# Optimization experiments

Measured on AMD Instinct MI355X. Metric: run time of the kernel, lower is better.

The kernel has to match this reference:

```python
import jax, jax.numpy as jnp
import numpy as np

D_MODEL = 1024
NHEAD = 16
HEAD_DIM = D_MODEL // NHEAD  # 64
AXIS_DIM = HEAD_DIM // 4     # 16
DFF = 4096
EPS = 1e-5
BASE = 10000.0
B, S = 4, 2048


def setup_inputs() -> dict:
    key = jax.random.key(0)
    ks = jax.random.split(key, 10)
    def xavier(k, shape):
        fan_in, fan_out = shape[1], shape[0]
        limit = np.sqrt(6.0 / (fan_in + fan_out))
        return jax.random.uniform(k, shape, jnp.float32, -limit, limit)
    return {
        "src": jax.random.normal(ks[0], (B, S, D_MODEL), jnp.float32),
        "positions": jax.random.normal(ks[1], (B, S, 4), jnp.float32),
        "w_qkv": xavier(ks[2], (3 * D_MODEL, D_MODEL)),
        "w_out": xavier(ks[3], (D_MODEL, D_MODEL)),
        "norm1_w": jnp.ones((D_MODEL,), jnp.float32),
        "norm2_w": jnp.ones((D_MODEL,), jnp.float32),
        "w1": xavier(ks[4], (DFF, D_MODEL)),
        "w2": xavier(ks[5], (D_MODEL, DFF)),
        "w3": xavier(ks[6], (DFF, D_MODEL)),
        "axis_scale": jnp.ones((4,), jnp.float32),
    }


def _rmsnorm(x, w, eps=EPS):
    return x * jax.lax.rsqrt(jnp.mean(x * x, axis=-1, keepdims=True) + eps) * w


def _rope_rotate(x, cos, sin):
    # x: (B,H,S,HEAD_DIM); cos/sin: (B,1,S,4,AXIS_DIM//2)
    b, h, s, _ = x.shape
    xr = x.reshape(b, h, s, 4, AXIS_DIM // 2, 2)  # 4 axis chunks, interleaved pairs
    e, o = xr[..., 0], xr[..., 1]
    re = e * cos - o * sin
    ro = o * cos + e * sin
    return jnp.stack([re, ro], axis=-1).reshape(b, h, s, HEAD_DIM)


def reference(src, positions, w_qkv, w_out, norm1_w, norm2_w, w1, w2, w3, axis_scale):
    b, s, _ = src.shape
    x = src
    x_norm = _rmsnorm(x, norm1_w)
    qkv = x_norm @ w_qkv.T  # (B,S,3*D)
    qkv = qkv.reshape(b, s, 3, NHEAD, HEAD_DIM).transpose(2, 0, 3, 1, 4)
    q, k, v = qkv[0], qkv[1], qkv[2]  # (B,H,S,Dh)

    # 4D RoPE: same inv_freq per axis (base^{-idx/axis_dim})
    inv_freq = BASE ** (-(jnp.arange(0, AXIS_DIM, 2, dtype=jnp.float32) / AXIS_DIM))  # (8,)
    coord = positions * axis_scale  # (B,S,4)
    angles = coord[..., None] * inv_freq  # (B,S,4,8)
    cos = jnp.cos(angles)[:, None]  # (B,1,S,4,8)
    sin = jnp.sin(angles)[:, None]
    q = _rope_rotate(q, cos, sin)
    k = _rope_rotate(k, cos, sin)

    scale = 1.0 / jnp.sqrt(jnp.float32(HEAD_DIM))
    scores = jnp.einsum("bhqd,bhkd->bhqk", q, k) * scale
    attn = jax.nn.softmax(scores, axis=-1)
    attn_out = jnp.einsum("bhqk,bhkd->bhqd", attn, v)
    attn_out = attn_out.transpose(0, 2, 1, 3).reshape(b, s, D_MODEL)
    x = x + attn_out @ w_out.T

    x_norm = _rmsnorm(x, norm2_w)
    ff = (jax.nn.silu(x_norm @ w1.T) * (x_norm @ w3.T)) @ w2.T
    return x + ff
```

## Files before the change

kernel.cpp:

```cpp
#include <hip/hip_runtime.h>

typedef unsigned short u16;
typedef __attribute__((ext_vector_type(4))) unsigned short u16x4;
typedef __attribute__((ext_vector_type(8))) short bf16x8;
typedef __attribute__((ext_vector_type(4))) float f32x4;
typedef __attribute__((ext_vector_type(16))) float f32x16;

__device__ __forceinline__ float bf2f(u16 u) {
  union { unsigned i; float f; } v; v.i = ((unsigned)u) << 16; return v.f;
}
__device__ __forceinline__ u16 f2bf(float f) {
  union { float f; unsigned i; } v; v.f = f;
  unsigned r = v.i + 0x7fffu + ((v.i >> 16) & 1u);
  return (u16)(r >> 16);
}
__device__ __forceinline__ void gl_lds16(const u16* g, u16* l) {
  __builtin_amdgcn_global_load_lds((const __attribute__((address_space(1))) unsigned*)g,
                                   (__attribute__((address_space(3))) unsigned*)l, 16, 0, 0);
}
__device__ __forceinline__ f32x16 mfma32(bf16x8 a, bf16x8 b, f32x16 c) {
  return __builtin_amdgcn_mfma_f32_32x32x16_bf16(a, b, c, 0, 0, 0);
}

__global__ __launch_bounds__(256) void k_cvt(const float* __restrict__ S,
                                             u16* __restrict__ D, int n) {
  int i = (blockIdx.x * 256 + threadIdx.x) * 8;
  if (i >= n) return;
  f32x4 a = *(const f32x4*)(S + i), b = *(const f32x4*)(S + i + 4);
  bf16x8 r;
  r[0] = (short)f2bf(a.x); r[1] = (short)f2bf(a.y); r[2] = (short)f2bf(a.z); r[3] = (short)f2bf(a.w);
  r[4] = (short)f2bf(b.x); r[5] = (short)f2bf(b.y); r[6] = (short)f2bf(b.z); r[7] = (short)f2bf(b.w);
  *(bf16x8*)(D + i) = r;
}

__global__ __launch_bounds__(256) void k_rmsnorm(const void* __restrict__ X,
                                                 const float* __restrict__ W,
                                                 u16* __restrict__ Y, int x_ext) {
  const int tok = blockIdx.x, t = threadIdx.x;
  float x0, x1, x2, x3;
  if (x_ext) {
    f32x4 xv = ((const f32x4*)X)[tok * 256 + t];
    x0 = xv.x; x1 = xv.y; x2 = xv.z; x3 = xv.w;
  } else {
    u16x4 xv = ((const u16x4*)X)[tok * 256 + t];
    x0 = bf2f(xv.x); x1 = bf2f(xv.y); x2 = bf2f(xv.z); x3 = bf2f(xv.w);
  }
  float ss = x0 * x0 + x1 * x1 + x2 * x2 + x3 * x3;
#pragma unroll
  for (int m = 32; m; m >>= 1) ss += __shfl_xor(ss, m);
  __shared__ float red[4];
  if ((t & 63) == 0) red[t >> 6] = ss;
  __syncthreads();
  float inv = rsqrtf((red[0] + red[1] + red[2] + red[3]) * (1.f / 1024.f) + 1e-5f);
  f32x4 wv = ((const f32x4*)W)[t];
  u16x4 o;
  o.x = f2bf(x0 * inv * wv.x);
  o.y = f2bf(x1 * inv * wv.y);
  o.z = f2bf(x2 * inv * wv.z);
  o.w = f2bf(x3 * inv * wv.w);
  ((u16x4*)(Y + (size_t)tok * 1024))[t] = o;
}

template <int EPI, int OUTF32>
__global__ __launch_bounds__(256, 2) void k_gemm(const u16* __restrict__ A,
                                                 const u16* __restrict__ W,
                                                 const void* R, void* C,
                                                 int M, int N, int K, int r_ext) {
  __shared__ u16 sA[128 * 32];
  __shared__ u16 sB[128 * 32];
  const int t = threadIdx.x;
  const int wid = t >> 6, lane = t & 63, quad = lane >> 4, l16 = lane & 15;
  const int wm = wid >> 1, wn = wid & 1;
  const size_t m0 = (size_t)blockIdx.y * 128, n0 = (size_t)blockIdx.x * 128;
  f32x4 acc[4][4] = {};
  const int srow = t >> 2, schunk = t & 3;
  const u16* Ag = A + (m0 + srow) * K + schunk * 8;
  const u16* Wg = W + (n0 + srow) * (size_t)K + schunk * 8;
  u16* sAw = sA + wid * 512;
  u16* sBw = sB + wid * 512;
  for (int k0 = 0; k0 < K; k0 += 32) {
    gl_lds16(Ag + k0, sAw);
    gl_lds16(Ag + (size_t)64 * K + k0, sAw + 2048);
    gl_lds16(Wg + k0, sBw);
    gl_lds16(Wg + (size_t)64 * K + k0, sBw + 2048);
    __syncthreads();
    bf16x8 a[4], b[4];
#pragma unroll
    for (int mt = 0; mt < 4; ++mt)
      a[mt] = *(const bf16x8*)(sA + (wm * 64 + mt * 16 + l16) * 32 + quad * 8);
#pragma unroll
    for (int nt = 0; nt < 4; ++nt)
      b[nt] = *(const bf16x8*)(sB + (wn * 64 + nt * 16 + l16) * 32 + quad * 8);
#pragma unroll
    for (int mt = 0; mt < 4; ++mt)
#pragma unroll
      for (int nt = 0; nt < 4; ++nt)
        acc[mt][nt] = __builtin_amdgcn_mfma_f32_16x16x32_bf16(a[mt], b[nt], acc[mt][nt], 0, 0, 0);
    __syncthreads();
  }
#pragma unroll
  for (int mt = 0; mt < 4; ++mt) {
#pragma unroll
    for (int nt = 0; nt < 4; ++nt) {
      size_t row = m0 + wm * 64 + mt * 16 + quad * 4;
      size_t col = n0 + wn * 64 + nt * 16 + l16;
#pragma unroll
      for (int r = 0; r < 4; ++r) {
        float v = acc[mt][nt][r];
        size_t idx = (row + r) * N + col;
        if (EPI == 1) v += r_ext ? ((const float*)R)[idx] : bf2f(((const u16*)R)[idx]);
        if (OUTF32) ((float*)C)[idx] = v;
        else ((u16*)C)[idx] = f2bf(v);
      }
    }
  }
}

__global__ __launch_bounds__(256, 2) void k_ffn(const u16* __restrict__ A,
                                                const u16* __restrict__ W1,
                                                const u16* __restrict__ W3,
                                                u16* __restrict__ C,
                                                int M, int N, int K) {
  __shared__ u16 sA[128 * 32];
  __shared__ u16 sB1[128 * 32];
  __shared__ u16 sB3[128 * 32];
  const int t = threadIdx.x;
  const int wid = t >> 6, lane = t & 63, quad = lane >> 4, l16 = lane & 15;
  const int wm = wid >> 1, wn = wid & 1;
  const size_t m0 = (size_t)blockIdx.y * 128, n0 = (size_t)blockIdx.x * 128;
  f32x4 acc1[4][4] = {};
  f32x4 acc3[4][4] = {};
  const int srow = t >> 2, schunk = t & 3;
  const u16* Ag = A + (m0 + srow) * K + schunk * 8;
  const u16* W1g = W1 + (n0 + srow) * (size_t)K + schunk * 8;
  const u16* W3g = W3 + (n0 + srow) * (size_t)K + schunk * 8;
  u16* sAw = sA + wid * 512;
  u16* sB1w = sB1 + wid * 512;
  u16* sB3w = sB3 + wid * 512;
  for (int k0 = 0; k0 < K; k0 += 32) {
    gl_lds16(Ag + k0, sAw);
    gl_lds16(Ag + (size_t)64 * K + k0, sAw + 2048);
    gl_lds16(W1g + k0, sB1w);
    gl_lds16(W1g + (size_t)64 * K + k0, sB1w + 2048);
    gl_lds16(W3g + k0, sB3w);
    gl_lds16(W3g + (size_t)64 * K + k0, sB3w + 2048);
    __syncthreads();
    bf16x8 a[4], b1[4], b3[4];
#pragma unroll
    for (int mt = 0; mt < 4; ++mt)
      a[mt] = *(const bf16x8*)(sA + (wm * 64 + mt * 16 + l16) * 32 + quad * 8);
#pragma unroll
    for (int nt = 0; nt < 4; ++nt) {
      b1[nt] = *(const bf16x8*)(sB1 + (wn * 64 + nt * 16 + l16) * 32 + quad * 8);
      b3[nt] = *(const bf16x8*)(sB3 + (wn * 64 + nt * 16 + l16) * 32 + quad * 8);
    }
#pragma unroll
    for (int mt = 0; mt < 4; ++mt)
#pragma unroll
      for (int nt = 0; nt < 4; ++nt) {
        acc1[mt][nt] = __builtin_amdgcn_mfma_f32_16x16x32_bf16(a[mt], b1[nt], acc1[mt][nt], 0, 0, 0);
        acc3[mt][nt] = __builtin_amdgcn_mfma_f32_16x16x32_bf16(a[mt], b3[nt], acc3[mt][nt], 0, 0, 0);
      }
    __syncthreads();
  }
#pragma unroll
  for (int mt = 0; mt < 4; ++mt) {
#pragma unroll
    for (int nt = 0; nt < 4; ++nt) {
      size_t row = m0 + wm * 64 + mt * 16 + quad * 4;
      size_t col = n0 + wn * 64 + nt * 16 + l16;
#pragma unroll
      for (int r = 0; r < 4; ++r) {
        float v1 = acc1[mt][nt][r];
        float v3 = acc3[mt][nt][r];
        float h = v1 / (1.f + __expf(-v1)) * v3;
        C[(row + r) * N + col] = f2bf(h);
      }
    }
  }
}

__global__ __launch_bounds__(256) void k_rope(const u16* __restrict__ QKV,
                                              const float* __restrict__ POS,
                                              const float* __restrict__ ASC,
                                              u16* __restrict__ Qr, u16* __restrict__ Kr,
                                              u16* __restrict__ Vt) {
  const int bh = blockIdx.x, b = bh >> 4, h = bh & 15;
  const int s0 = blockIdx.y * 128;
  const int t = threadIdx.x;
  const int pr = t & 31, a = pr >> 3, f = pr & 7, srow = t >> 5;
  const float asc = ASC[a];
  const float invf = exp2f(-(float)f * (13.28771237954945f / 8.f));
  for (int pass = 0; pass < 16; ++pass) {
    int s = s0 + pass * 8 + srow;
    float ang = POS[((size_t)b * 2048 + s) * 4 + a] * asc * invf;
    float sn, cs;
    sincosf(ang, &sn, &cs);
    size_t ib = ((size_t)b * 2048 + s) * 3072 + h * 64 + a * 16 + f * 2;
    size_t ob = ((size_t)bh * 2048 + s) * 64 + a * 16 + f * 2;
    unsigned qw = *(const unsigned*)(QKV + ib);
    float e = bf2f((u16)(qw & 0xffff)), o = bf2f((u16)(qw >> 16));
    *(unsigned*)(Qr + ob) = (unsigned)f2bf(e * cs - o * sn) | ((unsigned)f2bf(o * cs + e * sn) << 16);
    unsigned kw = *(const unsigned*)(QKV + ib + 1024);
    e = bf2f((u16)(kw & 0xffff));
    o = bf2f((u16)(kw >> 16));
    *(unsigned*)(Kr + ob) = (unsigned)f2bf(e * cs - o * sn) | ((unsigned)f2bf(o * cs + e * sn) << 16);
  }
  __shared__ u16 vt[64 * 130];
#pragma unroll
  for (int it = 0; it < 32; ++it) {
    int idx = it * 256 + t, sl = idx >> 6, d = idx & 63;
    vt[d * 130 + sl] = QKV[((size_t)b * 2048 + s0 + sl) * 3072 + 2048 + h * 64 + d];
  }
  __syncthreads();
#pragma unroll
  for (int it = 0; it < 32; ++it) {
    int idx = it * 256 + t, d = idx >> 7, sl = idx & 127;
    Vt[((size_t)bh * 64 + d) * 2048 + s0 + sl] = vt[d * 130 + sl];
  }
}

#define SCL 0.18033688011112042f

__global__ __launch_bounds__(256, 2) void k_attn(const u16* __restrict__ Qr,
                                                 const u16* __restrict__ Kr,
                                                 const u16* __restrict__ Vt,
                                                 u16* __restrict__ O) {
  __shared__ u16 sK[2][4096];
  __shared__ u16 sV[2][4096];
  const int t = threadIdx.x, wid = t >> 6, lane = t & 63;
  const int il = lane & 31, hh = lane >> 5;
  const int bh = blockIdx.x;
  const int q0 = blockIdx.y * 256 + wid * 64;
  const size_t base = (size_t)bh * 2048 * 64;

  bf16x8 qf[2][4];
#pragma unroll
  for (int qt = 0; qt < 2; ++qt)
#pragma unroll
    for (int c = 0; c < 4; ++c)
      qf[qt][c] = *(const bf16x8*)(Qr + base + (size_t)(q0 + qt * 32 + il) * 64 + c * 16 + hh * 8);

  const f32x16 ZERO = {};
  f32x16 oa[2][2] = {{ZERO, ZERO}, {ZERO, ZERO}};
  float m[2] = {-1e30f, -1e30f}, lr[2] = {0.f, 0.f};

  const u16* Kb = Kr + base;
  const u16* Vb = Vt + base;
  const int cc = t & 7, r0 = t >> 3;
  {
    bf16x8 k0 = *(const bf16x8*)(Kb + (size_t)r0 * 64 + cc * 8);
    bf16x8 k1 = *(const bf16x8*)(Kb + (size_t)(r0 + 32) * 64 + cc * 8);
    bf16x8 v0 = *(const bf16x8*)(Vb + (size_t)r0 * 2048 + cc * 8);
    bf16x8 v1 = *(const bf16x8*)(Vb + (size_t)(r0 + 32) * 2048 + cc * 8);
    *(bf16x8*)(sK[0] + (cc * 64 + (r0 ^ cc)) * 8) = k0;
    *(bf16x8*)(sK[0] + (cc * 64 + ((r0 + 32) ^ cc)) * 8) = k1;
    *(bf16x8*)(sV[0] + (cc * 64 + (r0 ^ cc)) * 8) = v0;
    *(bf16x8*)(sV[0] + (cc * 64 + ((r0 + 32) ^ cc)) * 8) = v1;
  }
  __syncthreads();

  for (int it = 0; it < 32; ++it) {
    const u16* kb = sK[it & 1];
    const u16* vb = sV[it & 1];
    bf16x8 nk0, nk1, nv0, nv1;
    const int last = (it == 31);
    if (!last) {
      int kv = (it + 1) * 64;
      nk0 = *(const bf16x8*)(Kb + (size_t)(kv + r0) * 64 + cc * 8);
      nk1 = *(const bf16x8*)(Kb + (size_t)(kv + r0 + 32) * 64 + cc * 8);
      nv0 = *(const bf16x8*)(Vb + (size_t)r0 * 2048 + kv + cc * 8);
      nv1 = *(const bf16x8*)(Vb + (size_t)(r0 + 32) * 2048 + kv + cc * 8);
    }
    f32x16 sacc[2][2];
    __builtin_amdgcn_s_setprio(1);
#pragma unroll
    for (int kt = 0; kt < 2; ++kt) {
#pragma unroll
      for (int c = 0; c < 4; ++c) {
        int ch = c * 2 + hh;
        bf16x8 kf = *(const bf16x8*)(kb + (ch * 64 + ((kt * 32 + il) ^ ch)) * 8);
        if (c == 0) {
          sacc[0][kt] = mfma32(kf, qf[0][0], ZERO);
          sacc[1][kt] = mfma32(kf, qf[1][0], ZERO);
        } else {
          sacc[0][kt] = mfma32(kf, qf[0][c], sacc[0][kt]);
          sacc[1][kt] = mfma32(kf, qf[1][c], sacc[1][kt]);
        }
      }
    }
    __builtin_amdgcn_s_setprio(0);
    bf16x8 pa[2][4];
#pragma unroll
    for (int qt = 0; qt < 2; ++qt) {
      float mx = -1e30f;
#pragma unroll
      for (int kt = 0; kt < 2; ++kt)
#pragma unroll
        for (int r = 0; r < 16; ++r) mx = fmaxf(mx, sacc[qt][kt][r]);
      mx = fmaxf(mx, __shfl_xor(mx, 32));
      if (!__all(mx - m[qt] <= 64.f)) {
        float mn = fmaxf(m[qt], mx);
        float corr = exp2f((m[qt] - mn) * SCL);
        m[qt] = mn;
        lr[qt] *= corr;
#pragma unroll
        for (int dt = 0; dt < 2; ++dt)
#pragma unroll
          for (int r = 0; r < 16; ++r) oa[qt][dt][r] *= corr;
      }
      float mm = m[qt];
#pragma unroll
      for (int kt = 0; kt < 2; ++kt) {
        float p[16];
        float ls = 0.f;
#pragma unroll
        for (int r = 0; r < 16; ++r) {
          p[r] = exp2f((sacc[qt][kt][r] - mm) * SCL);
          ls += p[r];
        }
        lr[qt] += ls;
        unsigned w[8];
#pragma unroll
        for (int i = 0; i < 8; ++i)
          asm("v_cvt_pk_bf16_f32 %0, %1, %2" : "=v"(w[i]) : "v"(p[2 * i]), "v"(p[2 * i + 1]));
        asm("v_permlane32_swap_b32 %0, %1" : "+v"(w[0]), "+v"(w[2]));
        asm("v_permlane32_swap_b32 %0, %1" : "+v"(w[1]), "+v"(w[3]));
        asm("v_permlane32_swap_b32 %0, %1" : "+v"(w[4]), "+v"(w[6]));
        asm("v_permlane32_swap_b32 %0, %1" : "+v"(w[5]), "+v"(w[7]));
        union { unsigned u[4]; bf16x8 v; } f0, f1;
        f0.u[0] = w[0]; f0.u[1] = w[1]; f0.u[2] = w[2]; f0.u[3] = w[3];
        f1.u[0] = w[4]; f1.u[1] = w[5]; f1.u[2] = w[6]; f1.u[3] = w[7];
        pa[qt][kt * 2] = f0.v;
        pa[qt][kt * 2 + 1] = f1.v;
      }
    }
    __builtin_amdgcn_s_setprio(1);
#pragma unroll
    for (int ks = 0; ks < 4; ++ks) {
      int sc = ks * 2 + hh;
#pragma unroll
      for (int dt = 0; dt < 2; ++dt) {
        bf16x8 vf = *(const bf16x8*)(vb + (sc * 64 + ((dt * 32 + il) ^ sc)) * 8);
        oa[0][dt] = mfma32(vf, pa[0][ks], oa[0][dt]);
        oa[1][dt] = mfma32(vf, pa[1][ks], oa[1][dt]);
      }
    }
    __builtin_amdgcn_s_setprio(0);
    if (!last) {
      u16* kn = sK[(it + 1) & 1];
      u16* vn = sV[(it + 1) & 1];
      *(bf16x8*)(kn + (cc * 64 + (r0 ^ cc)) * 8) = nk0;
      *(bf16x8*)(kn + (cc * 64 + ((r0 + 32) ^ cc)) * 8) = nk1;
      *(bf16x8*)(vn + (cc * 64 + (r0 ^ cc)) * 8) = nv0;
      *(bf16x8*)(vn + (cc * 64 + ((r0 + 32) ^ cc)) * 8) = nv1;
    }
    __syncthreads();
  }
  const int b = bh >> 4, hd = bh & 15;
#pragma unroll
  for (int qt = 0; qt < 2; ++qt) {
    float lt = lr[qt] + __shfl_xor(lr[qt], 32);
    float inv = 1.f / lt;
    int q = q0 + qt * 32 + il;
#pragma unroll
    for (int dt = 0; dt < 2; ++dt) {
#pragma unroll
      for (int g = 0; g < 4; ++g) {
        u16x4 pk;
        pk.x = f2bf(oa[qt][dt][4 * g + 0] * inv);
        pk.y = f2bf(oa[qt][dt][4 * g + 1] * inv);
        pk.z = f2bf(oa[qt][dt][4 * g + 2] * inv);
        pk.w = f2bf(oa[qt][dt][4 * g + 3] * inv);
        *(u16x4*)(O + ((size_t)b * 2048 + q) * 1024 + hd * 64 + dt * 32 + 8 * g + 4 * hh) = pk;
      }
    }
  }
}

extern "C" void kernel_launch(void* const* d_in, const int* in_sizes, int n_in,
                              void* d_out, int out_size, void* d_ws, size_t ws_size,
                              hipStream_t stream) {
  const float* src    = (const float*)d_in[0];
  const float* pos    = (const float*)d_in[1];
  const float* w_qkv  = (const float*)d_in[2];
  const float* w_out  = (const float*)d_in[3];
  const float* n1w    = (const float*)d_in[4];
  const float* n2w    = (const float*)d_in[5];
  const float* w1     = (const float*)d_in[6];
  const float* w2     = (const float*)d_in[7];
  const float* w3     = (const float*)d_in[8];
  const float* ascale = (const float*)d_in[9];
  char* ws = (char*)d_ws;
  u16* xn  = (u16*)(ws);
  u16* qkv = (u16*)(ws + ((size_t)16 << 20));
  u16* Qr  = (u16*)(ws);
  u16* Kr  = (u16*)(ws + ((size_t)64 << 20));
  u16* Vt  = (u16*)(ws + ((size_t)80 << 20));
  u16* att = (u16*)(ws + ((size_t)16 << 20));
  u16* x   = (u16*)(ws + ((size_t)80 << 20));
  u16* xn2 = (u16*)(ws);
  u16* h1  = (u16*)(ws + ((size_t)16 << 20));
  u16* bqkv = (u16*)(ws + ((size_t)96 << 20));
  u16* bout = (u16*)(ws + ((size_t)102 << 20));
  u16* b1   = (u16*)(ws + ((size_t)104 << 20));
  u16* b3   = (u16*)(ws + ((size_t)112 << 20));
  u16* b2   = (u16*)(ws + ((size_t)120 << 20));

  k_cvt<<<1536, 256, 0, stream>>>(w_qkv, bqkv, 3145728);
  k_cvt<<<512,  256, 0, stream>>>(w_out, bout, 1048576);
  k_cvt<<<2048, 256, 0, stream>>>(w1, b1, 4194304);
  k_cvt<<<2048, 256, 0, stream>>>(w3, b3, 4194304);
  k_cvt<<<2048, 256, 0, stream>>>(w2, b2, 4194304);

  k_rmsnorm<<<8192, 256, 0, stream>>>(src, n1w, xn, 1);
  k_gemm<0, 0><<<dim3(24, 64), 256, 0, stream>>>(xn, bqkv, nullptr, qkv, 8192, 3072, 1024, 0);
  k_rope<<<dim3(64, 16), 256, 0, stream>>>(qkv, pos, ascale, Qr, Kr, Vt);
  k_attn<<<dim3(64, 8), 256, 0, stream>>>(Qr, Kr, Vt, att);
  k_gemm<1, 0><<<dim3(8, 64), 256, 0, stream>>>(att, bout, src, x, 8192, 1024, 1024, 1);
  k_rmsnorm<<<8192, 256, 0, stream>>>(x, n2w, xn2, 0);
  k_ffn<<<dim3(32, 64), 256, 0, stream>>>(xn2, b1, b3, h1, 8192, 4096, 1024);
  k_gemm<1, 1><<<dim3(8, 64), 256, 0, stream>>>(h1, b2, x, d_out, 8192, 1024, 4096, 0);
}
```

Measured before the change: 699.5 us.

## Halve attention query tile per wave and reorganize GEMM LDS staging layout

The attention kernel now gives each wave 32 queries instead of 64 and launches twice as many blocks, raising the occupancy hint from 2 to 4 blocks per CU. The row max and row sum are now computed with tree reductions. The GEMM and FFN kernels change the global-to-LDS load mapping so that each wave stages whole 16-row MFMA tiles contiguously, which makes the fragment reads linear per lane and avoids strided LDS bank conflicts. The attention change trades fewer registers and more parallelism for half the reuse of each K/V tile per block, which means more LDS loads and K/V traffic.

```diff
diff --git a/kernel.cpp b/kernel.cpp
--- a/kernel.cpp
+++ b/kernel.cpp
@@ -73,9 +73,8 @@
   const int wm = wid >> 1, wn = wid & 1;
   const size_t m0 = (size_t)blockIdx.y * 128, n0 = (size_t)blockIdx.x * 128;
   f32x4 acc[4][4] = {};
-  const int srow = t >> 2, schunk = t & 3;
-  const u16* Ag = A + (m0 + srow) * K + schunk * 8;
-  const u16* Wg = W + (n0 + srow) * (size_t)K + schunk * 8;
+  const u16* Ag = A + (m0 + wid * 16 + l16) * (size_t)K + quad * 8;
+  const u16* Wg = W + (n0 + wid * 16 + l16) * (size_t)K + quad * 8;
   u16* sAw = sA + wid * 512;
   u16* sBw = sB + wid * 512;
   for (int k0 = 0; k0 < K; k0 += 32) {
@@ -87,10 +86,10 @@
     bf16x8 a[4], b[4];
 #pragma unroll
     for (int mt = 0; mt < 4; ++mt)
-      a[mt] = *(const bf16x8*)(sA + (wm * 64 + mt * 16 + l16) * 32 + quad * 8);
+      a[mt] = *(const bf16x8*)(sA + (wm * 4 + mt) * 512 + lane * 8);
 #pragma unroll
     for (int nt = 0; nt < 4; ++nt)
-      b[nt] = *(const bf16x8*)(sB + (wn * 64 + nt * 16 + l16) * 32 + quad * 8);
+      b[nt] = *(const bf16x8*)(sB + (wn * 4 + nt) * 512 + lane * 8);
 #pragma unroll
     for (int mt = 0; mt < 4; ++mt)
 #pragma unroll
@@ -130,10 +129,9 @@
   const size_t m0 = (size_t)blockIdx.y * 128, n0 = (size_t)blockIdx.x * 128;
   f32x4 acc1[4][4] = {};
   f32x4 acc3[4][4] = {};
-  const int srow = t >> 2, schunk = t & 3;
-  const u16* Ag = A + (m0 + srow) * K + schunk * 8;
-  const u16* W1g = W1 + (n0 + srow) * (size_t)K + schunk * 8;
-  const u16* W3g = W3 + (n0 + srow) * (size_t)K + schunk * 8;
+  const u16* Ag = A + (m0 + wid * 16 + l16) * (size_t)K + quad * 8;
+  const u16* W1g = W1 + (n0 + wid * 16 + l16) * (size_t)K + quad * 8;
+  const u16* W3g = W3 + (n0 + wid * 16 + l16) * (size_t)K + quad * 8;
   u16* sAw = sA + wid * 512;
   u16* sB1w = sB1 + wid * 512;
   u16* sB3w = sB3 + wid * 512;
@@ -148,11 +146,11 @@
     bf16x8 a[4], b1[4], b3[4];
 #pragma unroll
     for (int mt = 0; mt < 4; ++mt)
-      a[mt] = *(const bf16x8*)(sA + (wm * 64 + mt * 16 + l16) * 32 + quad * 8);
+      a[mt] = *(const bf16x8*)(sA + (wm * 4 + mt) * 512 + lane * 8);
 #pragma unroll
     for (int nt = 0; nt < 4; ++nt) {
-      b1[nt] = *(const bf16x8*)(sB1 + (wn * 64 + nt * 16 + l16) * 32 + quad * 8);
-      b3[nt] = *(const bf16x8*)(sB3 + (wn * 64 + nt * 16 + l16) * 32 + quad * 8);
+      b1[nt] = *(const bf16x8*)(sB1 + (wn * 4 + nt) * 512 + lane * 8);
+      b3[nt] = *(const bf16x8*)(sB3 + (wn * 4 + nt) * 512 + lane * 8);
     }
 #pragma unroll
     for (int mt = 0; mt < 4; ++mt)
@@ -222,7 +220,7 @@
 
 #define SCL 0.18033688011112042f
 
-__global__ __launch_bounds__(256, 2) void k_attn(const u16* __restrict__ Qr,
+__global__ __launch_bounds__(256, 4) void k_attn(const u16* __restrict__ Qr,
                                                  const u16* __restrict__ Kr,
                                                  const u16* __restrict__ Vt,
                                                  u16* __restrict__ O) {
@@ -231,19 +229,17 @@
   const int t = threadIdx.x, wid = t >> 6, lane = t & 63;
   const int il = lane & 31, hh = lane >> 5;
   const int bh = blockIdx.x;
-  const int q0 = blockIdx.y * 256 + wid * 64;
+  const int q0 = blockIdx.y * 128 + wid * 32;
   const size_t base = (size_t)bh * 2048 * 64;
 
-  bf16x8 qf[2][4];
-#pragma unroll
-  for (int qt = 0; qt < 2; ++qt)
-#pragma unroll
-    for (int c = 0; c < 4; ++c)
-      qf[qt][c] = *(const bf16x8*)(Qr + base + (size_t)(q0 + qt * 32 + il) * 64 + c * 16 + hh * 8);
+  bf16x8 qf[4];
+#pragma unroll
+  for (int c = 0; c < 4; ++c)
+    qf[c] = *(const bf16x8*)(Qr + base + (size_t)(q0 + il) * 64 + c * 16 + hh * 8);
 
   const f32x16 ZERO = {};
-  f32x16 oa[2][2] = {{ZERO, ZERO}, {ZERO, ZERO}};
-  float m[2] = {-1e30f, -1e30f}, lr[2] = {0.f, 0.f};
+  f32x16 oa[2] = {ZERO, ZERO};
+  float m = -1e30f, lr = 0.f;
 
   const u16* Kb = Kr + base;
   const u16* Vb = Vt + base;
@@ -272,7 +268,7 @@
       nv0 = *(const bf16x8*)(Vb + (size_t)r0 * 2048 + kv + cc * 8);
       nv1 = *(const bf16x8*)(Vb + (size_t)(r0 + 32) * 2048 + kv + cc * 8);
     }
-    f32x16 sacc[2][2];
+    f32x16 sacc[2];
     __builtin_amdgcn_s_setprio(1);
 #pragma unroll
     for (int kt = 0; kt < 2; ++kt) {
@@ -280,60 +276,54 @@
       for (int c = 0; c < 4; ++c) {
         int ch = c * 2 + hh;
         bf16x8 kf = *(const bf16x8*)(kb + (ch * 64 + ((kt * 32 + il) ^ ch)) * 8);
-        if (c == 0) {
-          sacc[0][kt] = mfma32(kf, qf[0][0], ZERO);
-          sacc[1][kt] = mfma32(kf, qf[1][0], ZERO);
-        } else {
-          sacc[0][kt] = mfma32(kf, qf[0][c], sacc[0][kt]);
-          sacc[1][kt] = mfma32(kf, qf[1][c], sacc[1][kt]);
-        }
+        sacc[kt] = (c == 0) ? mfma32(kf, qf[0], ZERO) : mfma32(kf, qf[c], sacc[kt]);
       }
     }
     __builtin_amdgcn_s_setprio(0);
-    bf16x8 pa[2][4];
-#pragma unroll
-    for (int qt = 0; qt < 2; ++qt) {
-      float mx = -1e30f;
-#pragma unroll
-      for (int kt = 0; kt < 2; ++kt)
-#pragma unroll
-        for (int r = 0; r < 16; ++r) mx = fmaxf(mx, sacc[qt][kt][r]);
-      mx = fmaxf(mx, __shfl_xor(mx, 32));
-      if (!__all(mx - m[qt] <= 64.f)) {
-        float mn = fmaxf(m[qt], mx);
-        float corr = exp2f((m[qt] - mn) * SCL);
-        m[qt] = mn;
-        lr[qt] *= corr;
-#pragma unroll
-        for (int dt = 0; dt < 2; ++dt)
-#pragma unroll
-          for (int r = 0; r < 16; ++r) oa[qt][dt][r] *= corr;
-      }
-      float mm = m[qt];
-#pragma unroll
-      for (int kt = 0; kt < 2; ++kt) {
-        float p[16];
-        float ls = 0.f;
-#pragma unroll
-        for (int r = 0; r < 16; ++r) {
-          p[r] = exp2f((sacc[qt][kt][r] - mm) * SCL);
-          ls += p[r];
-        }
-        lr[qt] += ls;
-        unsigned w[8];
-#pragma unroll
-        for (int i = 0; i < 8; ++i)
-          asm("v_cvt_pk_bf16_f32 %0, %1, %2" : "=v"(w[i]) : "v"(p[2 * i]), "v"(p[2 * i + 1]));
-        asm("v_permlane32_swap_b32 %0, %1" : "+v"(w[0]), "+v"(w[2]));
-        asm("v_permlane32_swap_b32 %0, %1" : "+v"(w[1]), "+v"(w[3]));
-        asm("v_permlane32_swap_b32 %0, %1" : "+v"(w[4]), "+v"(w[6]));
-        asm("v_permlane32_swap_b32 %0, %1" : "+v"(w[5]), "+v"(w[7]));
-        union { unsigned u[4]; bf16x8 v; } f0, f1;
-        f0.u[0] = w[0]; f0.u[1] = w[1]; f0.u[2] = w[2]; f0.u[3] = w[3];
-        f1.u[0] = w[4]; f1.u[1] = w[5]; f1.u[2] = w[6]; f1.u[3] = w[7];
-        pa[qt][kt * 2] = f0.v;
-        pa[qt][kt * 2 + 1] = f1.v;
-      }
+    float v[16];
+#pragma unroll
+    for (int r = 0; r < 16; ++r) v[r] = fmaxf(sacc[0][r], sacc[1][r]);
+#pragma unroll
+    for (int s = 8; s; s >>= 1)
+#pragma unroll
+      for (int r = 0; r < 8; ++r)
+        if (r < s) v[r] = fmaxf(v[r], v[r + s]);
+    float mx = fmaxf(v[0], __shfl_xor(v[0], 32));
+    if (!__all(mx - m <= 64.f)) {
+      float mn = fmaxf(m, mx);
+      float corr = exp2f((m - mn) * SCL);
+      m = mn;
+      lr *= corr;
+#pragma unroll
+      for (int dt = 0; dt < 2; ++dt)
+#pragma unroll
+        for (int r = 0; r < 16; ++r) oa[dt][r] *= corr;
+    }
+    bf16x8 pa[4];
+#pragma unroll
+    for (int kt = 0; kt < 2; ++kt) {
+      float p[16];
+#pragma unroll
+      for (int r = 0; r < 16; ++r) p[r] = exp2f((sacc[kt][r] - m) * SCL);
+      float s8[8];
+#pragma unroll
+      for (int r = 0; r < 8; ++r) s8[r] = p[r] + p[r + 8];
+      float s4a = (s8[0] + s8[4]) + (s8[1] + s8[5]);
+      float s4b = (s8[2] + s8[6]) + (s8[3] + s8[7]);
+      lr += s4a + s4b;
+      unsigned w[8];
+#pragma unroll
+      for (int i = 0; i < 8; ++i)
+        asm("v_cvt_pk_bf16_f32 %0, %1, %2" : "=v"(w[i]) : "v"(p[2 * i]), "v"(p[2 * i + 1]));
+      asm("v_permlane32_swap_b32 %0, %1" : "+v"(w[0]), "+v"(w[2]));
+      asm("v_permlane32_swap_b32 %0, %1" : "+v"(w[1]), "+v"(w[3]));
+      asm("v_permlane32_swap_b32 %0, %1" : "+v"(w[4]), "+v"(w[6]));
+      asm("v_permlane32_swap_b32 %0, %1" : "+v"(w[5]), "+v"(w[7]));
+      union { unsigned u[4]; bf16x8 v; } f0, f1;
+      f0.u[0] = w[0]; f0.u[1] = w[1]; f0.u[2] = w[2]; f0.u[3] = w[3];
+      f1.u[0] = w[4]; f1.u[1] = w[5]; f1.u[2] = w[6]; f1.u[3] = w[7];
+      pa[kt * 2] = f0.v;
+      pa[kt * 2 + 1] = f1.v;
     }
     __builtin_amdgcn_s_setprio(1);
 #pragma unroll
@@ -342,8 +332,7 @@
 #pragma unroll
       for (int dt = 0; dt < 2; ++dt) {
         bf16x8 vf = *(const bf16x8*)(vb + (sc * 64 + ((dt * 32 + il) ^ sc)) * 8);
-        oa[0][dt] = mfma32(vf, pa[0][ks], oa[0][dt]);
-        oa[1][dt] = mfma32(vf, pa[1][ks], oa[1][dt]);
+        oa[dt] = mfma32(vf, pa[ks], oa[dt]);
       }
     }
     __builtin_amdgcn_s_setprio(0);
@@ -358,20 +347,19 @@
     __syncthreads();
   }
   const int b = bh >> 4, hd = bh & 15;
-#pragma unroll
-  for (int qt = 0; qt < 2; ++qt) {
-    float lt = lr[qt] + __shfl_xor(lr[qt], 32);
+  {
+    float lt = lr + __shfl_xor(lr, 32);
     float inv = 1.f / lt;
-    int q = q0 + qt * 32 + il;
+    int q = q0 + il;
 #pragma unroll
     for (int dt = 0; dt < 2; ++dt) {
 #pragma unroll
       for (int g = 0; g < 4; ++g) {
         u16x4 pk;
-        pk.x = f2bf(oa[qt][dt][4 * g + 0] * inv);
-        pk.y = f2bf(oa[qt][dt][4 * g + 1] * inv);
-        pk.z = f2bf(oa[qt][dt][4 * g + 2] * inv);
-        pk.w = f2bf(oa[qt][dt][4 * g + 3] * inv);
+        pk.x = f2bf(oa[dt][4 * g + 0] * inv);
+        pk.y = f2bf(oa[dt][4 * g + 1] * inv);
+        pk.z = f2bf(oa[dt][4 * g + 2] * inv);
+        pk.w = f2bf(oa[dt][4 * g + 3] * inv);
         *(u16x4*)(O + ((size_t)b * 2048 + q) * 1024 + hd * 64 + dt * 32 + 8 * g + 4 * hh) = pk;
       }
     }
@@ -416,7 +404,7 @@
   k_rmsnorm<<<8192, 256, 0, stream>>>(src, n1w, xn, 1);
   k_gemm<0, 0><<<dim3(24, 64), 256, 0, stream>>>(xn, bqkv, nullptr, qkv, 8192, 3072, 1024, 0);
   k_rope<<<dim3(64, 16), 256, 0, stream>>>(qkv, pos, ascale, Qr, Kr, Vt);
-  k_attn<<<dim3(64, 8), 256, 0, stream>>>(Qr, Kr, Vt, att);
+  k_attn<<<dim3(64, 16), 256, 0, stream>>>(Qr, Kr, Vt, att);
   k_gemm<1, 0><<<dim3(8, 64), 256, 0, stream>>>(att, bout, src, x, 8192, 1024, 1024, 1);
   k_rmsnorm<<<8192, 256, 0, stream>>>(x, n2w, xn2, 0);
   k_ffn<<<dim3(32, 64), 256, 0, stream>>>(xn2, b1, b3, h1, 8192, 4096, 1024);
```

Result: slower. 814.5 us (+16.4%).
